# Performance work log

Hardware: AMD Instinct MI355X
Metric: run time of the kernel (lower is better)

The kernel has to match this reference:

```python
import jax, jax.numpy as jnp
import numpy as np

HOP = jnp.array([0, 1, 4, 7, 2, 5, 8, 3, 6, 9, 11, 14, 10, 12, 15, 13, 16])
GRAPH = jnp.array([0, 1, 4, 7, 2, 5, 8, 3, 6, 9, 12, 10, 13, 15, 11, 14, 16])
D_MODEL, L, D_INNER, D_STATE, DT_RANK = 512, 17, 1024, 4, 32


def layernorm(x, w, b, eps=1e-5):
    mu = x.mean(-1, keepdims=True)
    var = ((x - mu) ** 2).mean(-1, keepdims=True)
    return (x - mu) * jax.lax.rsqrt(var + eps) * w + b


def setup_inputs() -> dict:
    key = jax.random.key(0)
    ks = jax.random.split(key, 9)
    B = 4096
    s = lambda k, shape: jax.random.normal(k, shape, jnp.float32) * 0.02
    # A_log init per mamba_ssm: log(1..d_state) repeated over d_inner
    A_log = jnp.log(jnp.broadcast_to(jnp.arange(1, D_STATE + 1, dtype=jnp.float32), (D_INNER, D_STATE)))
    return {
        "x": jax.random.normal(ks[0], (B, L, D_MODEL), jnp.float32),
        "bp_embed": s(ks[1], (1, 5, D_MODEL)),
        "ln_w": jnp.ones((D_MODEL,), jnp.float32),
        "ln_b": jnp.zeros((D_MODEL,), jnp.float32),
        "in_proj_w": s(ks[2], (2 * D_INNER, D_MODEL)),
        "conv_w": 1.0 + s(ks[3], (D_INNER,)),  # d_conv=1 depthwise conv == per-channel scale
        "conv_b": jnp.zeros((D_INNER,), jnp.float32),
        "x_proj_w": s(ks[4], (DT_RANK + 2 * D_STATE, D_INNER)),
        "dt_proj_w": s(ks[5], (D_INNER, DT_RANK)),
        "dt_proj_b": s(ks[6], (D_INNER,)) - 4.0,  # softplus-inverse-ish small dt init
        "A_log": A_log,
        "D": jnp.ones((D_INNER,), jnp.float32),
        "out_proj_w": s(ks[7], (D_MODEL, D_INNER)),
    }


def mamba(u, in_proj_w, conv_w, conv_b, x_proj_w, dt_proj_w, dt_proj_b, A_log, D, out_proj_w):
    # u: [B, L, d_model]
    xz = jnp.einsum('bld,ed->ble', u, in_proj_w)          # [B,L,2*d_inner]
    xm, z = jnp.split(xz, 2, axis=-1)
    xm = jax.nn.silu(xm * conv_w + conv_b)                 # d_conv=1 -> pointwise
    x_dbl = jnp.einsum('ble,fe->blf', xm, x_proj_w)        # [B,L,dt_rank+2*d_state]
    dt_r = x_dbl[..., :DT_RANK]
    Bm = x_dbl[..., DT_RANK:DT_RANK + D_STATE]
    Cm = x_dbl[..., DT_RANK + D_STATE:]
    dt = jax.nn.softplus(jnp.einsum('blr,er->ble', dt_r, dt_proj_w) + dt_proj_b)  # [B,L,d_inner]
    A = -jnp.exp(A_log)                                    # [d_inner,d_state]

    def step(h, inp):
        dt_t, B_t, C_t, x_t = inp                          # [B,di],[B,ds],[B,ds],[B,di]
        dA = jnp.exp(dt_t[..., None] * A)                  # [B,di,ds]
        h = dA * h + (dt_t * x_t)[..., None] * B_t[:, None, :]
        y = jnp.einsum('bes,bs->be', h, C_t)
        return h, y

    bsz = u.shape[0]
    h0 = jnp.zeros((bsz, D_INNER, D_STATE), u.dtype)
    seq = (dt.transpose(1, 0, 2), Bm.transpose(1, 0, 2), Cm.transpose(1, 0, 2), xm.transpose(1, 0, 2))
    _, ys = jax.lax.scan(step, h0, seq)                    # ys: [L,B,d_inner]
    y = ys.transpose(1, 0, 2) + xm * D
    y = y * jax.nn.silu(z)
    return jnp.einsum('ble,de->bld', y, out_proj_w)


def reference(x, bp_embed, ln_w, ln_b, in_proj_w, conv_w, conv_b, x_proj_w,
              dt_proj_w, dt_proj_b, A_log, D, out_proj_w):
    bp = bp_embed
    x_bpe = jnp.concatenate([bp[:, :3], bp[:, :3], bp[:, :3], bp[:, :1],
                             bp[:, 3:], bp[:, :1], bp[:, 3:], bp[:, 3:]], axis=1)  # [1,17,dim]
    x_ssm = x[:, HOP, :] + x_bpe
    x_ssm = layernorm(x_ssm, ln_w, ln_b)
    x_ssm = mamba(x_ssm, in_proj_w, conv_w, conv_b, x_proj_w,
                  dt_proj_w, dt_proj_b, A_log, D, out_proj_w)
    return x + x_ssm[:, GRAPH, :]
```

## Files before the change

### kernel.cpp

```cpp
#include <hip/hip_runtime.h>

typedef unsigned short u16;
typedef unsigned int   u32;
typedef __bf16 bf16_t;
typedef bf16_t bf16x8 __attribute__((ext_vector_type(8)));
typedef float  f32x4  __attribute__((ext_vector_type(4)));

#define DEV static __device__ __forceinline__

__constant__ int c_HOP[17] = {0,1,4,7,2,5,8,3,6,9,11,14,10,12,15,13,16};
__constant__ int c_BPE[17] = {0,1,2,0,1,2,0,1,2,0,3,4,0,3,4,3,4};

DEV u16 f2bf(float f){
  u32 x = __builtin_bit_cast(u32, f);
  x += 0x7fffu + ((x >> 16) & 1u);
  return (u16)(x >> 16);
}
DEV float bf2f(u32 u){ return __builtin_bit_cast(float, u << 16); }
DEV float silu_f(float v){ return v / (1.f + __expf(-v)); }
DEV float softplus_f(float s){ return (s > 20.f) ? s : log1pf(__expf(s)); }

DEV void gll16(const void* g, void* l){
  __builtin_amdgcn_global_load_lds((__attribute__((address_space(1))) void*)g,
                                   (__attribute__((address_space(3))) void*)l,
                                   16, 0, 0);
}

__global__ __launch_bounds__(256) void cvt4(
    const float* __restrict__ s0, u16* __restrict__ d0, int n0,
    const float* __restrict__ s1, u16* __restrict__ d1, int n1,
    const float* __restrict__ s2, u16* __restrict__ d2, int n2,
    const float* __restrict__ s3, u16* __restrict__ d3, int n3)
{
  int t = blockIdx.x * 256 + threadIdx.x;
  if (t < n0){ d0[t] = f2bf(s0[t]); return; }
  t -= n0; if (t < n1){ d1[t] = f2bf(s1[t]); return; }
  t -= n1; if (t < n2){ d2[t] = f2bf(s2[t]); return; }
  t -= n2; if (t < n3){ d3[t] = f2bf(s3[t]); }
}

__global__ __launch_bounds__(256) void ln_gather(
    const float* __restrict__ x, const float* __restrict__ bpe,
    const float* __restrict__ lnw, const float* __restrict__ lnb,
    u16* __restrict__ u)
{
  int tok = blockIdx.x;
  int b = tok / 17;
  int l = tok - b * 17;
  const float* xr = x   + ((size_t)b * 17 + c_HOP[l]) * 512;
  const float* br = bpe + (size_t)c_BPE[l] * 512;
  int tid = threadIdx.x;
  int d0 = tid * 2;
  float2 xv = *(const float2*)(xr + d0);
  float2 bv = *(const float2*)(br + d0);
  float v0 = xv.x + bv.x, v1 = xv.y + bv.y;

  __shared__ float red[8];
  float s = v0 + v1;
  #pragma unroll
  for (int o = 32; o; o >>= 1) s += __shfl_xor(s, o);
  if ((tid & 63) == 0) red[tid >> 6] = s;
  __syncthreads();
  float mu = (red[0] + red[1] + red[2] + red[3]) * (1.f / 512.f);
  float a0 = v0 - mu, a1 = v1 - mu;
  float q = a0 * a0 + a1 * a1;
  #pragma unroll
  for (int o = 32; o; o >>= 1) q += __shfl_xor(q, o);
  if ((tid & 63) == 0) red[4 + (tid >> 6)] = q;
  __syncthreads();
  float var = (red[4] + red[5] + red[6] + red[7]) * (1.f / 512.f);
  float rs = rsqrtf(var + 1e-5f);

  u16 o0 = f2bf(a0 * rs * lnw[d0]     + lnb[d0]);
  u16 o1 = f2bf(a1 * rs * lnw[d0 + 1] + lnb[d0 + 1]);
  u32 pack = (u32)o0 | ((u32)o1 << 16);
  *(u32*)(u + (size_t)tok * 512 + d0) = pack;
}

enum { EPI_SPLIT = 0, EPI_XDBL = 1, EPI_OUT = 2 };

template<int EPI>
__global__ __launch_bounds__(256) void gemm_bt(
    const u16* __restrict__ A, int lda,
    const u16* __restrict__ W, int K, int MT,
    u16* __restrict__ ob0, u16* __restrict__ ob1,
    const float* __restrict__ p0, const float* __restrict__ p1,
    const float* __restrict__ xres, float* __restrict__ fout)
{
  __shared__ u16 sA[2][128 * 32];
  __shared__ u16 sW[2][128 * 32];
  int nwg = gridDim.x;
  int cpx = nwg >> 3;
  int wg = (blockIdx.x & 7) * cpx + (blockIdx.x >> 3);
  int NT = nwg / MT;
  int nt = wg % NT, mt = wg / NT;
  int brow = mt * 128, bcol = nt * 128;
  int tid = threadIdx.x, lane = tid & 63, wid = tid >> 6;
  int wm = wid >> 1, wn = wid & 1;

  f32x4 acc[4][4] = {};

  int srow = tid >> 2;
  int sch  = tid & 3;

  const u16* gA0 = A + (size_t)(brow + srow)      * lda + (sch ^ ((srow >> 1) & 3)) * 8;
  const u16* gA1 = A + (size_t)(brow + 64 + srow) * lda + (sch ^ (((64 + srow) >> 1) & 3)) * 8;
  const u16* gW0 = W + (size_t)(bcol + srow)      * K   + (sch ^ ((srow >> 1) & 3)) * 8;
  const u16* gW1 = W + (size_t)(bcol + 64 + srow) * K   + (sch ^ (((64 + srow) >> 1) & 3)) * 8;

  auto STAGE = [&](int buf, int kt) {
    gll16(gA0 + kt, (char*)sA[buf] + tid * 16);
    gll16(gA1 + kt, (char*)sA[buf] + tid * 16 + 4096);
    gll16(gW0 + kt, (char*)sW[buf] + tid * 16);
    gll16(gW1 + kt, (char*)sW[buf] + tid * 16 + 4096);
  };

  int aoff[4], boff[4];
  #pragma unroll
  for (int mi = 0; mi < 4; mi++) {
    int r = wm * 64 + mi * 16 + (lane & 15);
    int c = (lane >> 4) ^ ((r >> 1) & 3);
    aoff[mi] = r * 64 + c * 16;
  }
  #pragma unroll
  for (int ni = 0; ni < 4; ni++) {
    int r = wn * 64 + ni * 16 + (lane & 15);
    int c = (lane >> 4) ^ ((r >> 1) & 3);
    boff[ni] = r * 64 + c * 16;
  }

  auto COMPUTE = [&](int buf) {
    bf16x8 av[4], bv[4];
    #pragma unroll
    for (int mi = 0; mi < 4; mi++)
      av[mi] = *(const bf16x8*)((const char*)sA[buf] + aoff[mi]);
    #pragma unroll
    for (int ni = 0; ni < 4; ni++)
      bv[ni] = *(const bf16x8*)((const char*)sW[buf] + boff[ni]);
    #pragma unroll
    for (int mi = 0; mi < 4; mi++)
      #pragma unroll
      for (int ni = 0; ni < 4; ni++)
        acc[mi][ni] = __builtin_amdgcn_mfma_f32_16x16x32_bf16(
            av[mi], bv[ni], acc[mi][ni], 0, 0, 0);
  };

  int nsteps = K >> 5;
  STAGE(0, 0);
  __syncthreads();
  for (int s = 0; s < nsteps; s += 2) {
    if (s + 1 < nsteps) STAGE(1, (s + 1) << 5);
    COMPUTE(0);
    __syncthreads();
    if (s + 2 < nsteps) STAGE(0, (s + 2) << 5);
    COMPUTE(1);
    __syncthreads();
  }

  int r4 = (lane >> 4) * 4;
  int cl = lane & 15;
  #pragma unroll
  for (int mi = 0; mi < 4; mi++) {
    int rowb = brow + wm * 64 + mi * 16 + r4;
    #pragma unroll
    for (int ni = 0; ni < 4; ni++) {
      int col = bcol + wn * 64 + ni * 16 + cl;
      if constexpr (EPI == EPI_SPLIT) {
        bool isx = (col < 1024);
        float cw = isx ? p0[col] : 1.f;
        float cb = isx ? p1[col] : 0.f;
        u16* dst = isx ? (ob0 + col) : (ob1 + col - 1024);
        #pragma unroll
        for (int rr = 0; rr < 4; rr++)
          dst[(size_t)(rowb + rr) * 1024] = f2bf(silu_f(acc[mi][ni][rr] * cw + cb));
      } else if constexpr (EPI == EPI_XDBL) {
        if (col < 40) {
          #pragma unroll
          for (int rr = 0; rr < 4; rr++)
            ob0[(size_t)(rowb + rr) * 40 + col] = f2bf(acc[mi][ni][rr]);
        }
      } else {
        #pragma unroll
        for (int rr = 0; rr < 4; rr++) {
          int row = rowb + rr;
          u32 rw = (u32)row;
          u32 b = rw / 17u;
          int gl = (int)(rw - b * 17u);
          size_t oi = ((size_t)b * 17 + c_HOP[gl]) * 512 + col;
          fout[oi] = xres[oi] + acc[mi][ni][rr];
        }
      }
    }
  }
}

__global__ __launch_bounds__(128) void scan3(
    const u16* __restrict__ xm, const u16* __restrict__ zs,
    const u16* __restrict__ xdbl, const u16* __restrict__ wdt,
    const float* __restrict__ bdt, const float* __restrict__ A_log,
    const float* __restrict__ Dp, u16* __restrict__ y)
{
  __shared__ u16 xs[17 * 40];
  __shared__ u16 dt_s[17][520];

  int b = blockIdx.x;
  int tid = threadIdx.x, lane = tid & 63, wid = tid >> 6;
  int l15 = lane & 15, lhi = lane >> 4;
  const size_t base = (size_t)b * 17 * 1024;

  {
    const u32* src = (const u32*)(xdbl + (size_t)b * 680);
    for (int i = tid; i < 340; i += 128) ((u32*)xs)[i] = src[i];
  }
  __syncthreads();

  {
    bf16x8 a0 = *(const bf16x8*)(xs + l15 * 40 + lhi * 8);
    bf16x8 a1 = *(const bf16x8*)(xs + 16 * 40 + lhi * 8);
    #pragma unroll
    for (int nf = 0; nf < 32; nf++) {
      int e = wid * 512 + nf * 16 + l15;
      bf16x8 bv = *(const bf16x8*)(wdt + (size_t)e * 32 + lhi * 8);
      f32x4 c0 = {}, c1 = {};
      c0 = __builtin_amdgcn_mfma_f32_16x16x32_bf16(a0, bv, c0, 0, 0, 0);
      c1 = __builtin_amdgcn_mfma_f32_16x16x32_bf16(a1, bv, c1, 0, 0, 0);
      float bb = bdt[e];
      #pragma unroll
      for (int rr = 0; rr < 4; rr++) {
        int t = lhi * 4 + rr;
        dt_s[t][e] = f2bf(softplus_f(c0[rr] + bb));
      }
      if (lhi == 0) dt_s[16][e] = f2bf(softplus_f(c1[0] + bb));
    }
  }
  __syncthreads();

  {
    int e0 = tid * 8;
    float4 al = *(const float4*)(A_log + (size_t)e0 * 4);
    float A0 = -__expf(al.x), A1 = -__expf(al.y);
    float A2 = -__expf(al.z), A3 = -__expf(al.w);
    float Dv[8];
    *(float4*)(Dv)     = *(const float4*)(Dp + e0);
    *(float4*)(Dv + 4) = *(const float4*)(Dp + e0 + 4);

    const u16* xmb = xm + base + e0;
    const u16* zsb = zs + base + e0;
    u16* yb = y + base + e0;

    float h[8][4];
    #pragma unroll
    for (int c = 0; c < 8; c++)
      #pragma unroll
      for (int s = 0; s < 4; s++) h[c][s] = 0.f;

    #pragma unroll
    for (int t = 0; t < 17; t++) {
      uint4 xr = *(const uint4*)(xmb + t * 1024);
      uint4 zr = *(const uint4*)(zsb + t * 1024);
      uint4 dr = *(const uint4*)(&dt_s[t][e0]);
      uint4 bc = *(const uint4*)(xs + t * 40 + 32);
      float B0 = bf2f(bc.x & 0xffffu), B1 = bf2f(bc.x >> 16);
      float B2 = bf2f(bc.y & 0xffffu), B3 = bf2f(bc.y >> 16);
      float C0 = bf2f(bc.z & 0xffffu), C1 = bf2f(bc.z >> 16);
      float C2 = bf2f(bc.w & 0xffffu), C3 = bf2f(bc.w >> 16);
      u32 yo[4];
      const u32* xw = (const u32*)&xr;
      const u32* zw = (const u32*)&zr;
      const u32* dw = (const u32*)&dr;
      #pragma unroll
      for (int c = 0; c < 8; c++) {
        u32 x16 = (c & 1) ? (xw[c >> 1] >> 16) : (xw[c >> 1] & 0xffffu);
        u32 z16 = (c & 1) ? (zw[c >> 1] >> 16) : (zw[c >> 1] & 0xffffu);
        u32 d16 = (c & 1) ? (dw[c >> 1] >> 16) : (dw[c >> 1] & 0xffffu);
        float xv = bf2f(x16), zv = bf2f(z16), dtv = bf2f(d16);
        float dx = dtv * xv;
        h[c][0] = __expf(dtv * A0) * h[c][0] + dx * B0;
        h[c][1] = __expf(dtv * A1) * h[c][1] + dx * B1;
        h[c][2] = __expf(dtv * A2) * h[c][2] + dx * B2;
        h[c][3] = __expf(dtv * A3) * h[c][3] + dx * B3;
        float yv = h[c][0] * C0 + h[c][1] * C1 + h[c][2] * C2 + h[c][3] * C3;
        u16 pk = f2bf((yv + xv * Dv[c]) * zv);
        if (c & 1) yo[c >> 1] |= ((u32)pk << 16);
        else       yo[c >> 1] = (u32)pk;
      }
      *(uint4*)(yb + t * 1024) = *(uint4*)yo;
    }
  }
}

extern "C" void kernel_launch(void* const* d_in, const int* in_sizes, int n_in,
                              void* d_out, int out_size, void* d_ws, size_t ws_size,
                              hipStream_t stream) {
  const float* x     = (const float*)d_in[0];
  const float* bpe   = (const float*)d_in[1];
  const float* lnw   = (const float*)d_in[2];
  const float* lnb   = (const float*)d_in[3];
  const float* w_in  = (const float*)d_in[4];
  const float* convw = (const float*)d_in[5];
  const float* convb = (const float*)d_in[6];
  const float* w_xp  = (const float*)d_in[7];
  const float* w_dt  = (const float*)d_in[8];
  const float* b_dt  = (const float*)d_in[9];
  const float* A_log = (const float*)d_in[10];
  const float* Dp    = (const float*)d_in[11];
  const float* w_out = (const float*)d_in[12];
  float* out = (float*)d_out;

  u16* ws = (u16*)d_ws;
  u16* wb_in  = ws;
  u16* wb_out = wb_in  + 1048576;
  u16* wb_xp  = wb_out + 524288;
  u16* wb_dt  = wb_xp  + 40960;
  u16* xm     = wb_dt  + 32768;
  u16* zs     = xm     + 71303168;
  u16* xdbl   = zs     + 71303168;
  u16* yv     = xdbl   + 2785280;
  u16* u      = yv;

  const int MT = 544;

  cvt4<<<6432, 256, 0, stream>>>(w_in, wb_in, 1048576, w_out, wb_out, 524288,
                                 w_xp, wb_xp, 40960, w_dt, wb_dt, 32768);

  ln_gather<<<69632, 256, 0, stream>>>(x, bpe, lnw, lnb, u);

  gemm_bt<EPI_SPLIT><<<MT * 16, 256, 0, stream>>>(
      u, 512, wb_in, 512, MT, xm, zs, convw, convb, nullptr, nullptr);

  gemm_bt<EPI_XDBL><<<MT * 1, 256, 0, stream>>>(
      xm, 1024, wb_xp, 1024, MT, xdbl, nullptr, nullptr, nullptr, nullptr, nullptr);

  scan3<<<4096, 128, 0, stream>>>(xm, zs, xdbl, wb_dt, b_dt, A_log, Dp, yv);

  gemm_bt<EPI_OUT><<<MT * 4, 256, 0, stream>>>(
      yv, 1024, wb_out, 1024, MT, nullptr, nullptr, nullptr, nullptr, x, out);
}
```

Baseline: 899.3 us.

## Move dt projection out of scan into separate GEMM with softplus epilogue

The dt_proj matmul and softplus move out of the per-batch scan kernel into a standalone tiled GEMM (K=32) that writes dt to a bf16 buffer in global memory. The scan kernel then reads dt, B and C from global memory instead of building them in LDS, and writes y in place over the dt buffer. The GEMM loop gains a guard for an odd number of K steps. This drops the scan's LDS use and syncs, but adds a kernel launch and a full dt write and read through HBM (about 140MB of traffic).

```diff
diff --git a/kernel.cpp b/kernel.cpp
--- a/kernel.cpp
+++ b/kernel.cpp
@@ -77,7 +77,7 @@
   *(u32*)(u + (size_t)tok * 512 + d0) = pack;
 }
 
-enum { EPI_SPLIT = 0, EPI_XDBL = 1, EPI_OUT = 2 };
+enum { EPI_SPLIT = 0, EPI_XDBL = 1, EPI_DT = 2, EPI_OUT = 3 };
 
 template<int EPI>
 __global__ __launch_bounds__(256) void gemm_bt(
@@ -152,9 +152,11 @@
     if (s + 1 < nsteps) STAGE(1, (s + 1) << 5);
     COMPUTE(0);
     __syncthreads();
-    if (s + 2 < nsteps) STAGE(0, (s + 2) << 5);
-    COMPUTE(1);
-    __syncthreads();
+    if (s + 1 < nsteps) {
+      if (s + 2 < nsteps) STAGE(0, (s + 2) << 5);
+      COMPUTE(1);
+      __syncthreads();
+    }
   }
 
   int r4 = (lane >> 4) * 4;
@@ -179,6 +181,11 @@
           for (int rr = 0; rr < 4; rr++)
             ob0[(size_t)(rowb + rr) * 40 + col] = f2bf(acc[mi][ni][rr]);
         }
+      } else if constexpr (EPI == EPI_DT) {
+        float bb = p0[col];
+        #pragma unroll
+        for (int rr = 0; rr < 4; rr++)
+          ob0[(size_t)(rowb + rr) * 1024 + col] = f2bf(softplus_f(acc[mi][ni][rr] + bb));
       } else {
         #pragma unroll
         for (int rr = 0; rr < 4; rr++) {
@@ -194,98 +201,65 @@
   }
 }
 
-__global__ __launch_bounds__(128) void scan3(
+__global__ __launch_bounds__(128) void scan5(
     const u16* __restrict__ xm, const u16* __restrict__ zs,
-    const u16* __restrict__ xdbl, const u16* __restrict__ wdt,
-    const float* __restrict__ bdt, const float* __restrict__ A_log,
-    const float* __restrict__ Dp, u16* __restrict__ y)
+    const u16* __restrict__ xdbl, u16* __restrict__ dty,
+    const float* __restrict__ A_log, const float* __restrict__ Dp)
 {
-  __shared__ u16 xs[17 * 40];
-  __shared__ u16 dt_s[17][520];
-
   int b = blockIdx.x;
-  int tid = threadIdx.x, lane = tid & 63, wid = tid >> 6;
-  int l15 = lane & 15, lhi = lane >> 4;
+  int tid = threadIdx.x;
+  int e0 = tid * 8;
   const size_t base = (size_t)b * 17 * 1024;
 
-  {
-    const u32* src = (const u32*)(xdbl + (size_t)b * 680);
-    for (int i = tid; i < 340; i += 128) ((u32*)xs)[i] = src[i];
-  }
-  __syncthreads();
-
-  {
-    bf16x8 a0 = *(const bf16x8*)(xs + l15 * 40 + lhi * 8);
-    bf16x8 a1 = *(const bf16x8*)(xs + 16 * 40 + lhi * 8);
-    #pragma unroll
-    for (int nf = 0; nf < 32; nf++) {
-      int e = wid * 512 + nf * 16 + l15;
-      bf16x8 bv = *(const bf16x8*)(wdt + (size_t)e * 32 + lhi * 8);
-      f32x4 c0 = {}, c1 = {};
-      c0 = __builtin_amdgcn_mfma_f32_16x16x32_bf16(a0, bv, c0, 0, 0, 0);
-      c1 = __builtin_amdgcn_mfma_f32_16x16x32_bf16(a1, bv, c1, 0, 0, 0);
-      float bb = bdt[e];
-      #pragma unroll
-      for (int rr = 0; rr < 4; rr++) {
-        int t = lhi * 4 + rr;
-        dt_s[t][e] = f2bf(softplus_f(c0[rr] + bb));
-      }
-      if (lhi == 0) dt_s[16][e] = f2bf(softplus_f(c1[0] + bb));
+  float4 al = *(const float4*)(A_log + (size_t)e0 * 4);
+  float A0 = -__expf(al.x), A1 = -__expf(al.y);
+  float A2 = -__expf(al.z), A3 = -__expf(al.w);
+  float Dv[8];
+  *(float4*)(Dv)     = *(const float4*)(Dp + e0);
+  *(float4*)(Dv + 4) = *(const float4*)(Dp + e0 + 4);
+
+  const u16* xmb = xm + base + e0;
+  const u16* zsb = zs + base + e0;
+  u16* db = dty + base + e0;
+  const u16* bcb = xdbl + (size_t)b * 680 + 32;
+
+  float h[8][4];
+  #pragma unroll
+  for (int c = 0; c < 8; c++)
+    #pragma unroll
+    for (int s = 0; s < 4; s++) h[c][s] = 0.f;
+
+  #pragma unroll
+  for (int t = 0; t < 17; t++) {
+    uint4 xr = *(const uint4*)(xmb + t * 1024);
+    uint4 zr = *(const uint4*)(zsb + t * 1024);
+    uint4 dr = *(const uint4*)(db + t * 1024);
+    uint4 bc = *(const uint4*)(bcb + t * 40);
+    float B0 = bf2f(bc.x & 0xffffu), B1 = bf2f(bc.x >> 16);
+    float B2 = bf2f(bc.y & 0xffffu), B3 = bf2f(bc.y >> 16);
+    float C0 = bf2f(bc.z & 0xffffu), C1 = bf2f(bc.z >> 16);
+    float C2 = bf2f(bc.w & 0xffffu), C3 = bf2f(bc.w >> 16);
+    u32 yo[4];
+    const u32* xw = (const u32*)&xr;
+    const u32* zw = (const u32*)&zr;
+    const u32* dw = (const u32*)&dr;
+    #pragma unroll
+    for (int c = 0; c < 8; c++) {
+      u32 x16 = (c & 1) ? (xw[c >> 1] >> 16) : (xw[c >> 1] & 0xffffu);
+      u32 z16 = (c & 1) ? (zw[c >> 1] >> 16) : (zw[c >> 1] & 0xffffu);
+      u32 d16 = (c & 1) ? (dw[c >> 1] >> 16) : (dw[c >> 1] & 0xffffu);
+      float xv = bf2f(x16), zv = bf2f(z16), dtv = bf2f(d16);
+      float dx = dtv * xv;
+      h[c][0] = __expf(dtv * A0) * h[c][0] + dx * B0;
+      h[c][1] = __expf(dtv * A1) * h[c][1] + dx * B1;
+      h[c][2] = __expf(dtv * A2) * h[c][2] + dx * B2;
+      h[c][3] = __expf(dtv * A3) * h[c][3] + dx * B3;
+      float yv = h[c][0] * C0 + h[c][1] * C1 + h[c][2] * C2 + h[c][3] * C3;
+      u16 pk = f2bf((yv + xv * Dv[c]) * zv);
+      if (c & 1) yo[c >> 1] |= ((u32)pk << 16);
+      else       yo[c >> 1] = (u32)pk;
     }
-  }
-  __syncthreads();
-
-  {
-    int e0 = tid * 8;
-    float4 al = *(const float4*)(A_log + (size_t)e0 * 4);
-    float A0 = -__expf(al.x), A1 = -__expf(al.y);
-    float A2 = -__expf(al.z), A3 = -__expf(al.w);
-    float Dv[8];
-    *(float4*)(Dv)     = *(const float4*)(Dp + e0);
-    *(float4*)(Dv + 4) = *(const float4*)(Dp + e0 + 4);
-
-    const u16* xmb = xm + base + e0;
-    const u16* zsb = zs + base + e0;
-    u16* yb = y + base + e0;
-
-    float h[8][4];
-    #pragma unroll
-    for (int c = 0; c < 8; c++)
-      #pragma unroll
-      for (int s = 0; s < 4; s++) h[c][s] = 0.f;
-
-    #pragma unroll
-    for (int t = 0; t < 17; t++) {
-      uint4 xr = *(const uint4*)(xmb + t * 1024);
-      uint4 zr = *(const uint4*)(zsb + t * 1024);
-      uint4 dr = *(const uint4*)(&dt_s[t][e0]);
-      uint4 bc = *(const uint4*)(xs + t * 40 + 32);
-      float B0 = bf2f(bc.x & 0xffffu), B1 = bf2f(bc.x >> 16);
-      float B2 = bf2f(bc.y & 0xffffu), B3 = bf2f(bc.y >> 16);
-      float C0 = bf2f(bc.z & 0xffffu), C1 = bf2f(bc.z >> 16);
-      float C2 = bf2f(bc.w & 0xffffu), C3 = bf2f(bc.w >> 16);
-      u32 yo[4];
-      const u32* xw = (const u32*)&xr;
-      const u32* zw = (const u32*)&zr;
-      const u32* dw = (const u32*)&dr;
-      #pragma unroll
-      for (int c = 0; c < 8; c++) {
-        u32 x16 = (c & 1) ? (xw[c >> 1] >> 16) : (xw[c >> 1] & 0xffffu);
-        u32 z16 = (c & 1) ? (zw[c >> 1] >> 16) : (zw[c >> 1] & 0xffffu);
-        u32 d16 = (c & 1) ? (dw[c >> 1] >> 16) : (dw[c >> 1] & 0xffffu);
-        float xv = bf2f(x16), zv = bf2f(z16), dtv = bf2f(d16);
-        float dx = dtv * xv;
-        h[c][0] = __expf(dtv * A0) * h[c][0] + dx * B0;
-        h[c][1] = __expf(dtv * A1) * h[c][1] + dx * B1;
-        h[c][2] = __expf(dtv * A2) * h[c][2] + dx * B2;
-        h[c][3] = __expf(dtv * A3) * h[c][3] + dx * B3;
-        float yv = h[c][0] * C0 + h[c][1] * C1 + h[c][2] * C2 + h[c][3] * C3;
-        u16 pk = f2bf((yv + xv * Dv[c]) * zv);
-        if (c & 1) yo[c >> 1] |= ((u32)pk << 16);
-        else       yo[c >> 1] = (u32)pk;
-      }
-      *(uint4*)(yb + t * 1024) = *(uint4*)yo;
-    }
+    *(uint4*)(db + t * 1024) = *(uint4*)yo;
   }
 }
 
@@ -315,8 +289,8 @@
   u16* xm     = wb_dt  + 32768;
   u16* zs     = xm     + 71303168;
   u16* xdbl   = zs     + 71303168;
-  u16* yv     = xdbl   + 2785280;
-  u16* u      = yv;
+  u16* dty    = xdbl   + 2785280;
+  u16* u      = dty;
 
   const int MT = 544;
 
@@ -331,8 +305,11 @@
   gemm_bt<EPI_XDBL><<<MT * 1, 256, 0, stream>>>(
       xm, 1024, wb_xp, 1024, MT, xdbl, nullptr, nullptr, nullptr, nullptr, nullptr);
 
-  scan3<<<4096, 128, 0, stream>>>(xm, zs, xdbl, wb_dt, b_dt, A_log, Dp, yv);
+  gemm_bt<EPI_DT><<<MT * 8, 256, 0, stream>>>(
+      xdbl, 40, wb_dt, 32, MT, dty, nullptr, b_dt, nullptr, nullptr, nullptr);
+
+  scan5<<<4096, 128, 0, stream>>>(xm, zs, xdbl, dty, A_log, Dp);
 
   gemm_bt<EPI_OUT><<<MT * 4, 256, 0, stream>>>(
-      yv, 1024, wb_out, 1024, MT, nullptr, nullptr, nullptr, nullptr, x, out);
-}
+      dty, 1024, wb_out, 1024, MT, nullptr, nullptr, nullptr, nullptr, x, out);
+}
```

New measurement: 985.3 us. +9.6%, slower.
